# Kernel tuning notes

Measured on AMD Instinct MI355X. Metric: run time of the kernel, lower is better.

The kernel has to match this reference:

```python
import jax, jax.numpy as jnp
import numpy as np

_R, _C = 64, 64
_N = _R * _C
_SEC_PER_A = 31556926.0
_K = 0.01        # sheet_conductivity
_ALPHA = 1.25    # sheet_flow_exp
_HR = 0.1        # bedrock_step_height
_LR = 2.0        # cavity_spacing
_A = 5e-25       # cavity_closure_coeff
_NEXP = 3        # Glen exponent


def _build_grid():
    idx = np.arange(_N).reshape(_R, _C)
    tail = np.concatenate([idx[:, :-1].ravel(), idx[:-1, :].ravel()]).astype(np.int32)
    head = np.concatenate([idx[:, 1:].ravel(), idx[1:, :].ravel()]).astype(np.int32)
    L = tail.size
    links_at_node = -np.ones((_N, 4), np.int32)
    adj = -np.ones((_N, 4), np.int32)
    cnt = np.zeros(_N, np.int32)
    for l in range(L):
        for a, b in ((tail[l], head[l]), (head[l], tail[l])):
            links_at_node[a, cnt[a]] = l
            adj[a, cnt[a]] = b
            cnt[a] += 1
    r, c = np.divmod(np.arange(_N), _C)
    status = ((r == 0) | (r == _R - 1) | (c == 0) | (c == _C - 1)).astype(np.int32)
    return tail, head, links_at_node, adj, status


def setup_inputs():
    key = jax.random.key(0)
    k = jax.random.split(key, 8)
    tail, head, links_at_node, adj, status = _build_grid()
    L = tail.size
    bedrock = jax.random.uniform(k[0], (_N,), jnp.float32, 0.0, 500.0)
    ice_thk = jax.random.uniform(k[1], (_N,), jnp.float32, 100.0, 1000.0)
    overburden = 917.0 * 9.81 * ice_thk
    base_potential = 1000.0 * 9.81 * bedrock + overburden
    potential = base_potential - 0.3 * overburden + 1e3 * jax.random.normal(k[2], (_N,), jnp.float32)
    sheet_thickness = jax.random.uniform(k[3], (_N,), jnp.float32, 0.01, 0.1)
    sliding_velocity = jax.random.uniform(k[4], (L,), jnp.float32, 10.0, 100.0)
    specific_melt_rate = jax.random.uniform(k[5], (_N,), jnp.float32, 1e-7, 1e-6)
    link_length = jnp.full((L,), 100.0, jnp.float32)
    adj_j = jnp.asarray(adj)
    # mean over ALL 4 slots, padded entries contribute 0 (matches original jnp.mean)
    adj_pot = jnp.mean(jnp.where(adj_j != -1, base_potential[adj_j], 0.0), axis=1)
    inflow = jnp.where(base_potential > adj_pot, 1, -1) * (jnp.asarray(status) > 0)
    return dict(
        base_potential=base_potential,
        overburden_pressure=overburden,
        specific_melt_rate=specific_melt_rate,
        sheet_thickness=sheet_thickness,
        potential=potential,
        sliding_velocity=sliding_velocity,
        link_length=link_length,
        link_tail=jnp.asarray(tail),
        link_head=jnp.asarray(head),
        links_at_node=jnp.asarray(links_at_node),
        inflow_outflow=inflow.astype(jnp.int32),
        dt=3600,
    )


def reference(base_potential, overburden_pressure, specific_melt_rate, sheet_thickness,
              potential, sliding_velocity, link_length, link_tail, link_head,
              links_at_node, inflow_outflow, dt):
    N = base_potential.shape[0]
    t, h = link_tail, link_head
    # --- elliptic operator assembly (per-link, scatter into dense [N,N]) ---
    sheets = 0.5 * (sheet_thickness[t] + sheet_thickness[h])
    inv_grad = jnp.abs((potential[t] - potential[h]) / link_length) ** (-0.5)
    c = -_K * sheets ** _ALPHA * link_length * inv_grad  # symmetric link coefficient (<0)
    dir_row = inflow_outflow == 1  # Dirichlet rows
    ct = jnp.where(dir_row[t], 0.0, c)  # contribution into row tail
    ch = jnp.where(dir_row[h], 0.0, c)  # contribution into row head
    M = (jnp.zeros((N, N), base_potential.dtype)
         .at[t, h].add(ct).at[h, t].add(ch)
         .at[t, t].add(-ct).at[h, h].add(-ch))
    M = jnp.where(dir_row[:, None], jnp.eye(N, dtype=M.dtype), M)
    forcing = jnp.where(dir_row, base_potential - overburden_pressure, specific_melt_rate)
    new_potential = jnp.linalg.solve(M, forcing)
    # --- sheet thickness: map_mean_of_links_to_node then Newton on node-local ODE ---
    valid = links_at_node != -1
    lv = (sliding_velocity / _SEC_PER_A)[links_at_node]  # [N,4]
    sliding = jnp.abs(jnp.sum(jnp.where(valid, lv, 0.0), axis=1)
                      / jnp.maximum(valid.sum(axis=1), 1))
    pressure = base_potential - new_potential
    dtf = jnp.asarray(dt, base_potential.dtype)
    # residual r(h) = h - h0 - dt*(sliding*(HR-h)/LR - A*P^n*h) is LINEAR in h,
    # so Newton converges in one exact step -> closed form:
    new_h = (sheet_thickness + dtf * sliding * _HR / _LR) / (
        1.0 + dtf * (sliding / _LR + _A * pressure ** _NEXP))
    return new_potential, new_h
```

## Files before the change

### kernel.cpp

```cpp
#include <hip/hip_runtime.h>
#include <math.h>


#define NT    512
#define NPT   8
#define NN    4096
#define NC    1024
#define NCC   256
#define CCIT  20
#define MAXIT 40

enum : int { RSHL1 = 0x101, RSHR1 = 0x111,
             ROR8 = 0x128, ROR12 = 0x12C, ROR14 = 0x12E, ROR15 = 0x12F,
             WSHL1 = 0x130, WSHR1 = 0x138 };

template<int CTRL>
__device__ __forceinline__ float dppf(float x) {
    return __int_as_float(__builtin_amdgcn_update_dpp(
        __float_as_int(x), __float_as_int(x), CTRL, 0xF, 0xF, false));
}
template<int CTRL>
__device__ __forceinline__ double dppd(double x) {
    const int lo = __double2loint(x), hi = __double2hiint(x);
    const int l2 = __builtin_amdgcn_update_dpp(lo, lo, CTRL, 0xF, 0xF, false);
    const int h2 = __builtin_amdgcn_update_dpp(hi, hi, CTRL, 0xF, 0xF, false);
    return __hiloint2double(h2, l2);
}
__device__ __forceinline__ void pl16sw(int& a, int& b) {
    asm volatile("s_nop 1\n\tv_permlane16_swap_b32 %0, %1" : "+v"(a), "+v"(b));
}
__device__ __forceinline__ void pl32sw(int& a, int& b) {
    asm volatile("s_nop 1\n\tv_permlane32_swap_b32 %0, %1" : "+v"(a), "+v"(b));
}
__device__ __forceinline__ float shift_dn16(float x, bool inR2) {
    int a = __float_as_int(x), b = __float_as_int(x);
    pl16sw(a, b);
    int g = b, g2 = b;
    pl32sw(g, g2);
    return __int_as_float(inR2 ? g : a);
}
__device__ __forceinline__ float shift_up16(float x, bool inR1) {
    int a = __float_as_int(x), b = __float_as_int(x);
    pl16sw(a, b);
    int d1 = __float_as_int(x), d2 = __float_as_int(x);
    pl32sw(d1, d2);
    int e1 = d2, e2 = d2;
    pl16sw(e1, e2);
    return __int_as_float(inR1 ? e1 : b);
}
__device__ __forceinline__ double dsw32(double x) {
    int lo = __double2loint(x), hi = __double2hiint(x);
    int a = lo, b = lo; pl32sw(a, b);
    int c = hi, d = hi; pl32sw(c, d);
    return __hiloint2double(d, b);
}
__device__ __forceinline__ double dsw16(double x) {
    int lo = __double2loint(x), hi = __double2hiint(x);
    int a = lo, b = lo; pl16sw(a, b);
    int c = hi, d = hi; pl16sw(c, d);
    return __hiloint2double(d, b);
}

__global__ __launch_bounds__(NT, 1)
void sds_solver(const float* __restrict__ base_pot,
                const float* __restrict__ ovb,
                const float* __restrict__ melt,
                const float* __restrict__ sheet,
                const float* __restrict__ pot,
                const float* __restrict__ svel,
                const float* __restrict__ llen,
                const int*   __restrict__ ltail,
                const int*   __restrict__ lhead,
                const int*   __restrict__ lan,
                const int*   __restrict__ inflow,
                const int*   __restrict__ dt_raw,
                float* __restrict__ out,
                int N, int L)
{
    __shared__ __align__(16) float ZL0[2112], ZH0[2112];
    __shared__ __align__(16) float ZL1[2112], ZH1[2112];
    __shared__ __align__(16) float cW[NN], cE[NN], cN[NN], cS[NN];
    __shared__ __align__(16) float CB[32 + NC + 32];
    __shared__ __align__(16) float CB2[32 + NC + 32];
    __shared__ __align__(16) float EB[32 + NC + 32];
    __shared__ __align__(16) float ccb[NCC];
    __shared__ __align__(16) float cWc_s[NC], cEc_s[NC], cNc_s[NC], cSc_s[NC], dc_s[NC];
    __shared__ double redp[32], redg[16];

    const int tid  = threadIdx.x;
    const int lane = tid & 63;
    const int wid  = tid >> 6;
    const int m    = tid * NPT;

    if (N != NN || L != 8064) return;

    const int dti = dt_raw[0];
    const float as_f = __int_as_float(dti);
    const double dtf = (as_f > 0.5f && as_f < 1.0e12f) ? (double)as_f : (double)dti;

    const float invthf = 0.8f;
    const float c1f = 0.2195122f, c2f = 0.9756098f;
    const float wA = 1.75f;

    {
        const float4 z4 = make_float4(0.f, 0.f, 0.f, 0.f);
        #pragma unroll
        for (int i = tid; i < NN/4; i += NT) {
            ((float4*)cW)[i] = z4; ((float4*)cE)[i] = z4;
            ((float4*)cN)[i] = z4; ((float4*)cS)[i] = z4;
        }
        if (tid < 32) {
            ZL0[tid]=0.f; ZL0[2080+tid]=0.f; ZH0[tid]=0.f; ZH0[2080+tid]=0.f;
            ZL1[tid]=0.f; ZL1[2080+tid]=0.f; ZH1[tid]=0.f; ZH1[2080+tid]=0.f;
            CB[tid]=0.f;  CB[32+NC+tid]=0.f;
            CB2[tid]=0.f; CB2[32+NC+tid]=0.f;
            EB[tid]=0.f;  EB[32+NC+tid]=0.f;
        }
    }
    __syncthreads();

    for (int l = tid; l < 8064; l += NT) {
        int t, h;
        if (l < 4032) {
            const int r = l / 63;
            const int c2 = l - r * 63;
            t = (r << 6) + c2; h = t + 1;
        } else {
            t = l - 4032; h = t + 64;
        }
        const float sheets = 0.5f * (sheet[t] + sheet[h]);
        const float len = llen[l];
        const float grad = fabsf((pot[t] - pot[h]) / len);
        const float c = -0.01f * (sheets * sqrtf(sqrtf(sheets))) * len / sqrtf(grad);
        const bool dt_ = (inflow[t] == 1);
        const bool dh_ = (inflow[h] == 1);
        if (l < 4032) { cE[t] = dt_ ? 0.f : c; cW[h] = dh_ ? 0.f : c; }
        else          { cS[t] = dt_ ? 0.f : c; cN[h] = dh_ ? 0.f : c; }
    }
    __syncthreads();

    float cw[NPT], ce[NPT], cn[NPT], cs[NPT], dgf[NPT], invdf[NPT];
    double bb[NPT], gg[NPT], xv[NPT], rv[NPT];
    bool dirf[NPT];
    auto ldco = [&]() {
        const float4 w0 = *(const float4*)&cW[m], w1 = *(const float4*)&cW[m+4];
        const float4 e0 = *(const float4*)&cE[m], e1 = *(const float4*)&cE[m+4];
        const float4 n0 = *(const float4*)&cN[m], n1 = *(const float4*)&cN[m+4];
        const float4 s0 = *(const float4*)&cS[m], s1 = *(const float4*)&cS[m+4];
        cw[0]=w0.x;cw[1]=w0.y;cw[2]=w0.z;cw[3]=w0.w;cw[4]=w1.x;cw[5]=w1.y;cw[6]=w1.z;cw[7]=w1.w;
        ce[0]=e0.x;ce[1]=e0.y;ce[2]=e0.z;ce[3]=e0.w;ce[4]=e1.x;ce[5]=e1.y;ce[6]=e1.z;ce[7]=e1.w;
        cn[0]=n0.x;cn[1]=n0.y;cn[2]=n0.z;cn[3]=n0.w;cn[4]=n1.x;cn[5]=n1.y;cn[6]=n1.z;cn[7]=n1.w;
        cs[0]=s0.x;cs[1]=s0.y;cs[2]=s0.z;cs[3]=s0.w;cs[4]=s1.x;cs[5]=s1.y;cs[6]=s1.z;cs[7]=s1.w;
    };
    ldco();
    double gsum = 0.0, gcnt = 0.0;
    #pragma unroll
    for (int k = 0; k < NPT; ++k) {
        const int n = m + k;
        const bool dir = (inflow[n] == 1);
        const double g = (double)base_pot[n] - (double)ovb[n];
        const double d = -((double)cw[k] + (double)ce[k] + (double)cn[k] + (double)cs[k]);
        const double dg = (dir || d == 0.0) ? 1.0 : d;
        dgf[k] = (float)dg; invdf[k] = (float)(1.0 / dg);
        bb[k] = dir ? g : (double)melt[n];
        gg[k] = g; dirf[k] = dir;
        if (dir) { gsum += g; gcnt += 1.0; }
    }
    {
        #pragma unroll
        for (int off = 32; off > 0; off >>= 1) {
            gsum += __shfl_down(gsum, off, 64);
            gcnt += __shfl_down(gcnt, off, 64);
        }
        if (lane == 0) { redg[2*wid] = gsum; redg[2*wid+1] = gcnt; }
        __syncthreads();
        gsum = 0.0; gcnt = 0.0;
        #pragma unroll
        for (int w = 0; w < NT/64; ++w) { gsum += redg[2*w]; gcnt += redg[2*w+1]; }
    }
    const double gmean = gsum / (gcnt > 0.0 ? gcnt : 1.0);

    auto stz = [&](float* L_, float* H_, const float* v) {
        *(float4*)&L_[32 + 4*tid] = make_float4(v[0], v[1], v[2], v[3]);
        *(float4*)&H_[32 + 4*tid] = make_float4(v[4], v[5], v[6], v[7]);
    };
    float qf[NPT];
    auto spmv = [&](const float* L_, const float* H_, const float* vr) {
        const float4 uL = *(const float4*)&L_[4*tid];
        const float4 uH = *(const float4*)&H_[4*tid];
        const float4 dL = *(const float4*)&L_[64 + 4*tid];
        const float4 dH = *(const float4*)&H_[64 + 4*tid];
        const float lw = dppf<WSHR1>(vr[7]);
        const float re = dppf<WSHL1>(vr[0]);
        const float up[NPT] = {uL.x,uL.y,uL.z,uL.w,uH.x,uH.y,uH.z,uH.w};
        const float dn[NPT] = {dL.x,dL.y,dL.z,dL.w,dH.x,dH.y,dH.z,dH.w};
        #pragma unroll
        for (int k = 0; k < NPT; ++k) {
            const float wv = k ? vr[k-1] : lw;
            const float ev = (k < NPT-1) ? vr[k+1] : re;
            qf[k] = dgf[k]*vr[k] + cw[k]*wv + ce[k]*ev + cn[k]*up[k] + cs[k]*dn[k];
        }
    };
    auto fread0 = [&](int n) -> float {
        const int off = 32 + ((n >> 3) << 2) + (n & 3);
        return (n & 4) ? ZH0[off] : ZL0[off];
    };

    {
        float x0r[NPT];
        #pragma unroll
        for (int k = 0; k < NPT; ++k) {
            const float x0f = (float)(dirf[k] ? gg[k] : gmean);
            xv[k] = (double)x0f; x0r[k] = x0f;
        }
        stz(ZL0, ZH0, x0r); __syncthreads();
        spmv(ZL0, ZH0, x0r);
        #pragma unroll
        for (int k = 0; k < NPT; ++k)
            rv[k] = dirf[k] ? 0.0 : (bb[k] - (double)qf[k]);
    }
    __syncthreads();

    {
        #pragma unroll
        for (int k = 0; k < NPT; ++k) {
            const int n = m + k;
            if ((n & 63) != 0  && inflow[n-1]  == 1) cW[n] = 0.f;
            if ((n & 63) != 63 && inflow[n+1]  == 1) cE[n] = 0.f;
            if (n >= 64        && inflow[n-64] == 1) cN[n] = 0.f;
            if (n < NN-64      && inflow[n+64] == 1) cS[n] = 0.f;
        }
        float dgfF[NPT];
        #pragma unroll
        for (int k = 0; k < NPT; ++k) dgfF[k] = dirf[k] ? 0.f : dgf[k];
        stz(ZL0, ZH0, dgfF);
    }
    __syncthreads();
    ldco();

    #pragma unroll
    for (int q = 0; q < 2; ++q) {
        const int I = 2*tid + q;
        const int R = tid >> 4, C = I & 31;
        const int na = 128*R + 2*C, nb = na+1, nc_ = na+64, nd = na+65;
        cEc_s[I] = cE[nb] + cE[nd];
        cWc_s[I] = cW[na] + cW[nc_];
        cNc_s[I] = cN[na] + cN[nb];
        cSc_s[I] = cS[nc_] + cS[nd];
        const float d = fread0(na)+fread0(nb)+fread0(nc_)+fread0(nd)
                      + 2.0f*(cE[na] + cE[nc_] + cS[na] + cS[nb]);
        dc_s[I] = (d > 0.f) ? d : 1.0f;
    }
    __syncthreads();

    float cwc[2], cec[2], cnc[2], csc[2], dcr[2], invdc[2];
    {
        float2 t;
        t = *(float2*)&cWc_s[2*tid]; cwc[0]=t.x; cwc[1]=t.y;
        t = *(float2*)&cEc_s[2*tid]; cec[0]=t.x; cec[1]=t.y;
        t = *(float2*)&cNc_s[2*tid]; cnc[0]=t.x; cnc[1]=t.y;
        t = *(float2*)&cSc_s[2*tid]; csc[0]=t.x; csc[1]=t.y;
        t = *(float2*)&dc_s[2*tid];  dcr[0]=t.x; dcr[1]=t.y;
        invdc[0] = 1.0f/dcr[0]; invdc[1] = 1.0f/dcr[1];
    }
    float cwcc[4], cecc[4], cncc[4], cscc[4], dccr[4], invdcc[4];
    if (tid < 64) {
        #pragma unroll
        for (int j = 0; j < 4; ++j) {
            const int Rc = ((tid >> 4) << 2) + j, Cc = tid & 15;
            const int IA = 64*Rc + 2*Cc, IB = IA+1, IC = IA+32, ID = IA+33;
            cecc[j] = cEc_s[IB] + cEc_s[ID];
            cwcc[j] = cWc_s[IA] + cWc_s[IC];
            cncc[j] = cNc_s[IA] + cNc_s[IB];
            cscc[j] = cSc_s[IC] + cSc_s[ID];
            const float d = dc_s[IA]+dc_s[IB]+dc_s[IC]+dc_s[ID]
                          + 2.0f*(cEc_s[IA] + cEc_s[IC] + cSc_s[IA] + cSc_s[IB]);
            dccr[j] = (d > 0.f) ? d : 1.0f;
            invdcc[j] = 1.0f/dccr[j];
        }
    }
    float c1cc[CCIT+1], c2cc[CCIT+1], invthcc;
    {
        const double a = 8e-3, b2 = 2.0;
        const double th = 0.5*(b2+a), de = 0.5*(b2-a), s1 = th/de;
        double rp = 1.0/s1;
        for (int j = 1; j <= CCIT; ++j) {
            const double rj = 1.0/(2.0*s1 - rp);
            c1cc[j] = (float)(rj*rp);
            c2cc[j] = (float)(2.0*rj/de);
            rp = rj;
        }
        invthcc = (float)(1.0/th);
    }
    auto cspmv = [&](const float* B_, float v0, float v1, float& q0, float& q1) {
        const float2 up = *(const float2*)&B_[2*tid];
        const float2 dn = *(const float2*)&B_[64 + 2*tid];
        const float wv = dppf<WSHR1>(v1);
        const float ev = dppf<WSHL1>(v0);
        q0 = dcr[0]*v0 + cwc[0]*wv + cec[0]*v1 + cnc[0]*up.x + csc[0]*dn.x;
        q1 = dcr[1]*v1 + cwc[1]*v0 + cec[1]*ev + cnc[1]*up.y + csc[1]*dn.y;
    };

    double rho_prev = 0.0, pap = 0.0, tol = 0.0;
    double pv[NPT], sv[NPT], rpv[NPT];
    #pragma unroll
    for (int k = 0; k < NPT; ++k) { pv[k]=0.0; sv[k]=0.0; rpv[k]=0.0; }

    for (int it = 0; it < MAXIT; ++it) {
        float f0[NPT], d0[NPT], d1[NPT], zpre[NPT];
        #pragma unroll
        for (int k = 0; k < NPT; ++k) { f0[k] = (float)rv[k] * invdf[k]; d0[k] = f0[k] * invthf; }
        stz(ZL0, ZH0, d0); __syncthreads();
        spmv(ZL0, ZH0, d0);
        #pragma unroll
        for (int k = 0; k < NPT; ++k) {
            const float f1 = f0[k] - qf[k]*invdf[k];
            d1[k] = c1f*d0[k] + c2f*f1;
            zpre[k] = d0[k] + d1[k];
            f0[k] = f1;
        }
        stz(ZL1, ZH1, d1); __syncthreads();
        spmv(ZL1, ZH1, d1);

        float r1[NPT], r1p[NPT];
        #pragma unroll
        for (int k = 0; k < NPT; ++k) {
            const float fres = f0[k] - qf[k]*invdf[k];
            r1[k] = dirf[k] ? 0.f : dgf[k]*fres;
        }
        #pragma unroll
        for (int k = 0; k < NPT; ++k) r1p[k] = dppf<ROR8>(r1[k]);
        if ((tid & 8) == 0) {
            float4 rc4;
            rc4.x = r1[0]+r1[1]+r1p[0]+r1p[1];
            rc4.y = r1[2]+r1[3]+r1p[2]+r1p[3];
            rc4.z = r1[4]+r1[5]+r1p[4]+r1p[5];
            rc4.w = r1[6]+r1[7]+r1p[6]+r1p[7];
            const int I0 = 32*(tid >> 4) + 4*(tid & 7);
            *(float4*)&CB2[32 + I0] = rc4;
        }
        __syncthreads();

        float rc[2], f0c[2], d0c[2], d1c[2], qc0, qc1;
        {
            const float2 rcl = *(const float2*)&CB2[32 + 2*tid];
            rc[0] = rcl.x; rc[1] = rcl.y;
        }
        #pragma unroll
        for (int q = 0; q < 2; ++q) {
            f0c[q] = rc[q] * invdc[q];
            d0c[q] = f0c[q] * invthf;
        }
        *(float2*)&CB[32 + 2*tid] = make_float2(d0c[0], d0c[1]);
        __syncthreads();
        cspmv(CB, d0c[0], d0c[1], qc0, qc1);
        {
            const float f1a = f0c[0] - qc0*invdc[0];
            const float f1b = f0c[1] - qc1*invdc[1];
            d1c[0] = c1f*d0c[0] + c2f*f1a;
            d1c[1] = c1f*d0c[1] + c2f*f1b;
            f0c[0] = f1a; f0c[1] = f1b;
        }
        *(float2*)&CB2[32 + 2*tid] = make_float2(d1c[0], d1c[1]);
        __syncthreads();
        cspmv(CB2, d1c[0], d1c[1], qc0, qc1);
        {
            const float fra = f0c[0] - qc0*invdc[0];
            const float frb = f0c[1] - qc1*invdc[1];
            *(float2*)&CB[32 + 2*tid] = make_float2(dcr[0]*fra, dcr[1]*frb);
        }
        __syncthreads();

        if (tid < 64) {
            const int cc_c  = tid & 15;
            const int cc_rb = tid >> 4;
            const bool inR1 = (cc_rb == 1), inR2 = (cc_rb == 2);
            float fr[4], dr[4], zc[4];
            #pragma unroll
            for (int j = 0; j < 4; ++j) {
                const int IA = (((cc_rb << 2) + j) << 6) + (cc_c << 1);
                const float rcc = CB[32+IA] + CB[32+IA+1] + CB[32+IA+32] + CB[32+IA+33];
                fr[j] = rcc * invdcc[j];
                dr[j] = fr[j] * invthcc;
                zc[j] = dr[j];
            }
            for (int s = 1; s <= CCIT; ++s) {
                const float zN = shift_dn16(dr[3], inR2);
                const float zS = shift_up16(dr[0], inR1);
                float qcc[4];
                #pragma unroll
                for (int j = 0; j < 4; ++j) {
                    const float wj = dppf<RSHR1>(dr[j]);
                    const float ej = dppf<RSHL1>(dr[j]);
                    const float nj = j ? dr[j-1] : zN;
                    const float sj = (j < 3) ? dr[j+1] : zS;
                    qcc[j] = dccr[j]*dr[j] + cwcc[j]*wj + cecc[j]*ej
                           + cncc[j]*nj + cscc[j]*sj;
                }
                #pragma unroll
                for (int j = 0; j < 4; ++j) {
                    fr[j] -= qcc[j] * invdcc[j];
                    dr[j]  = c1cc[s]*dr[j] + c2cc[s]*fr[j];
                    zc[j] += dr[j];
                }
            }
            #pragma unroll
            for (int j = 0; j < 4; ++j)
                ccb[(((cc_rb << 2) + j) << 4) + cc_c] = zc[j];
        }
        __syncthreads();

        const float ecv = wA * ccb[16*(tid >> 5) + (tid & 15)];
        float zmc[2] = { d0c[0] + d1c[0] + ecv, d0c[1] + d1c[1] + ecv };
        *(float2*)&CB2[32 + 2*tid] = make_float2(zmc[0], zmc[1]);
        __syncthreads();
        cspmv(CB2, zmc[0], zmc[1], qc0, qc1);
        float fmc[2] = { (rc[0]-qc0)*invdc[0], (rc[1]-qc1)*invdc[1] };
        float d0p[2] = { fmc[0]*invthf, fmc[1]*invthf };
        *(float2*)&CB[32 + 2*tid] = make_float2(d0p[0], d0p[1]);
        __syncthreads();
        cspmv(CB, d0p[0], d0p[1], qc0, qc1);
        {
            const float f1a = fmc[0] - qc0*invdc[0];
            const float f1b = fmc[1] - qc1*invdc[1];
            const float efa = zmc[0] + c1f*d0p[0] + c2f*f1a + d0p[0];
            const float efb = zmc[1] + c1f*d0p[1] + c2f*f1b + d0p[1];
            *(float2*)&EB[32 + 2*tid] = make_float2(efa, efb);
        }
        __syncthreads();

        const float4 e4 = *(const float4*)&EB[32 + 32*(tid >> 4) + (tid & 7)*4];
        const float* e4p = (const float*)&e4;
        float zmid[NPT], zf[NPT];
        #pragma unroll
        for (int k = 0; k < NPT; ++k)
            zmid[k] = zpre[k] + (dirf[k] ? 0.f : wA * e4p[k >> 1]);
        stz(ZL1, ZH1, zmid); __syncthreads();
        spmv(ZL1, ZH1, zmid);
        float fmid[NPT], d0q[NPT];
        #pragma unroll
        for (int k = 0; k < NPT; ++k) {
            fmid[k] = (float)rv[k]*invdf[k] - qf[k]*invdf[k];
            d0q[k]  = fmid[k] * invthf;
        }
        stz(ZL0, ZH0, d0q); __syncthreads();
        spmv(ZL0, ZH0, d0q);
        #pragma unroll
        for (int k = 0; k < NPT; ++k) {
            const float f1 = fmid[k] - qf[k]*invdf[k];
            zf[k] = zmid[k] + d0q[k] + c1f*d0q[k] + c2f*f1;
        }
        stz(ZL1, ZH1, zf); __syncthreads();
        spmv(ZL1, ZH1, zf);

        double rho_n = 0.0, rzp = 0.0, zw = 0.0, pw = 0.0;
        #pragma unroll
        for (int k = 0; k < NPT; ++k) {
            const double zk = (double)zf[k], wk = (double)qf[k];
            rho_n += rv[k]  * zk;
            rzp   += rpv[k] * zk;
            zw    += zk * wk;
            pw    += pv[k] * wk;
        }
        rho_n += dsw32(rho_n); rzp += dsw32(rzp); zw += dsw32(zw); pw += dsw32(pw);
        rho_n += dsw16(rho_n); rzp += dsw16(rzp); zw += dsw16(zw); pw += dsw16(pw);
        rho_n += dppd<ROR8 >(rho_n); rzp += dppd<ROR8 >(rzp); zw += dppd<ROR8 >(zw); pw += dppd<ROR8 >(pw);
        rho_n += dppd<ROR12>(rho_n); rzp += dppd<ROR12>(rzp); zw += dppd<ROR12>(zw); pw += dppd<ROR12>(pw);
        rho_n += dppd<ROR14>(rho_n); rzp += dppd<ROR14>(rzp); zw += dppd<ROR14>(zw); pw += dppd<ROR14>(pw);
        rho_n += dppd<ROR15>(rho_n); rzp += dppd<ROR15>(rzp); zw += dppd<ROR15>(zw); pw += dppd<ROR15>(pw);
        if (lane == 0) {
            redp[4*wid] = rho_n; redp[4*wid+1] = rzp;
            redp[4*wid+2] = zw;  redp[4*wid+3] = pw;
        }
        __syncthreads();
        rho_n = 0.0; rzp = 0.0; zw = 0.0; pw = 0.0;
        #pragma unroll
        for (int w = 0; w < NT/64; ++w) {
            rho_n += redp[4*w];   rzp += redp[4*w+1];
            zw    += redp[4*w+2]; pw  += redp[4*w+3];
        }

        if (it == 0) {
            tol = rho_n * 1e-3 + 1e-300;
            if (!(rho_n > 0.0)) break;
        } else if (rho_n <= tol || !(rho_n > 0.0)) break;
        const double beta = (it == 0) ? 0.0
                          : fmax(0.0, (rho_n - rzp) / rho_prev);
        pap = zw + beta * (2.0 * pw + beta * pap);
        if (!(pap > 0.0)) break;
        const double alpha = rho_n / pap;
        rho_prev = rho_n;
        #pragma unroll
        for (int k = 0; k < NPT; ++k) {
            rpv[k] = rv[k];
            pv[k] = (double)zf[k] + beta * pv[k];
            sv[k] = (double)qf[k] + beta * sv[k];
            xv[k] += alpha * pv[k];
            rv[k] -= alpha * sv[k];
        }
    }

    float xo[NPT], ho[NPT];
    #pragma unroll
    for (int k = 0; k < NPT; ++k) {
        const int n = m + k;
        const int r = n >> 6, c2 = n & 63;
        const double x = dirf[k] ? gg[k] : xv[k];
        xo[k] = (float)x;

        const int hb = r * 63 + c2;
        float sva = 0.0f; int cnt = 0;
        if (c2 > 0)  { sva += svel[hb - 1];       cnt++; }
        if (c2 < 63) { sva += svel[hb];           cnt++; }
        if (r  > 0)  { sva += svel[4032 + n - 64]; cnt++; }
        if (r  < 63) { sva += svel[4032 + n];      cnt++; }
        const double sliding =
            fabs((double)sva / 31556926.0 / (double)(cnt > 0 ? cnt : 1));
        const double P   = (double)base_pot[n] - x;
        const double num = (double)sheet[n] + dtf * sliding * 0.1 / 2.0;
        const double den = 1.0 + dtf * (sliding / 2.0 + 5e-25 * P * P * P);
        ho[k] = (float)(num / den);
    }
    *(float4*)&out[m]        = make_float4(xo[0], xo[1], xo[2], xo[3]);
    *(float4*)&out[m+4]      = make_float4(xo[4], xo[5], xo[6], xo[7]);
    *(float4*)&out[NN+m]     = make_float4(ho[0], ho[1], ho[2], ho[3]);
    *(float4*)&out[NN+m+4]   = make_float4(ho[4], ho[5], ho[6], ho[7]);
}

extern "C" void kernel_launch(void* const* d_in, const int* in_sizes, int n_in,
                              void* d_out, int out_size, void* d_ws, size_t ws_size,
                              hipStream_t stream) {
    const float* base_pot = (const float*)d_in[0];
    const float* ovb      = (const float*)d_in[1];
    const float* melt     = (const float*)d_in[2];
    const float* sheet    = (const float*)d_in[3];
    const float* pot      = (const float*)d_in[4];
    const float* svel     = (const float*)d_in[5];
    const float* llen     = (const float*)d_in[6];
    const int*   ltail    = (const int*)d_in[7];
    const int*   lhead    = (const int*)d_in[8];
    const int*   lan      = (const int*)d_in[9];
    const int*   inflow   = (const int*)d_in[10];
    const int*   dt_raw   = (const int*)d_in[11];
    float* out = (float*)d_out;
    const int N = in_sizes[0];
    const int L = in_sizes[5];

    hipLaunchKernelGGL(sds_solver, dim3(1), dim3(NT), 0, stream,
                       base_pot, ovb, melt, sheet, pot, svel, llen,
                       ltail, lhead, lan, inflow, dt_raw, out, N, L);
}
```

Measured before the change: 149.4 us.

## Recompute neighbor halo values locally to drop barrier-separated SpMV staging

```diff
diff --git a/kernel.cpp b/kernel.cpp
--- a/kernel.cpp
+++ b/kernel.cpp
@@ -79,10 +79,12 @@
 {
     __shared__ __align__(16) float ZL0[2112], ZH0[2112];
     __shared__ __align__(16) float ZL1[2112], ZH1[2112];
+    __shared__ __align__(16) float DML[2112], DMH[2112];
     __shared__ __align__(16) float cW[NN], cE[NN], cN[NN], cS[NN];
     __shared__ __align__(16) float CB[32 + NC + 32];
     __shared__ __align__(16) float CB2[32 + NC + 32];
     __shared__ __align__(16) float EB[32 + NC + 32];
+    __shared__ __align__(16) float IDC[32 + NC + 32];
     __shared__ __align__(16) float ccb[NCC];
     __shared__ __align__(16) float cWc_s[NC], cEc_s[NC], cNc_s[NC], cSc_s[NC], dc_s[NC];
     __shared__ double redp[32], redg[16];
@@ -112,9 +114,11 @@
         if (tid < 32) {
             ZL0[tid]=0.f; ZL0[2080+tid]=0.f; ZH0[tid]=0.f; ZH0[2080+tid]=0.f;
             ZL1[tid]=0.f; ZL1[2080+tid]=0.f; ZH1[tid]=0.f; ZH1[2080+tid]=0.f;
+            DML[tid]=0.f; DML[2080+tid]=0.f; DMH[tid]=0.f; DMH[2080+tid]=0.f;
             CB[tid]=0.f;  CB[32+NC+tid]=0.f;
             CB2[tid]=0.f; CB2[32+NC+tid]=0.f;
             EB[tid]=0.f;  EB[32+NC+tid]=0.f;
+            IDC[tid]=0.f; IDC[32+NC+tid]=0.f;
         }
     }
     __syncthreads();
@@ -184,6 +188,12 @@
         *(float4*)&L_[32 + 4*tid] = make_float4(v[0], v[1], v[2], v[3]);
         *(float4*)&H_[32 + 4*tid] = make_float4(v[4], v[5], v[6], v[7]);
     };
+    {
+        float dmf[NPT];
+        #pragma unroll
+        for (int k = 0; k < NPT; ++k) dmf[k] = dirf[k] ? 0.f : 1.f;
+        stz(DML, DMH, dmf);
+    }
     float qf[NPT];
     auto spmv = [&](const float* L_, const float* H_, const float* vr) {
         const float4 uL = *(const float4*)&L_[4*tid];
@@ -262,6 +272,7 @@
         t = *(float2*)&cSc_s[2*tid]; csc[0]=t.x; csc[1]=t.y;
         t = *(float2*)&dc_s[2*tid];  dcr[0]=t.x; dcr[1]=t.y;
         invdc[0] = 1.0f/dcr[0]; invdc[1] = 1.0f/dcr[1];
+        *(float2*)&IDC[32 + 2*tid] = make_float2(invdc[0], invdc[1]);
     }
     float cwcc[4], cecc[4], cncc[4], cscc[4], dccr[4], invdcc[4];
     if (tid < 64) {
@@ -351,9 +362,18 @@
             f0c[q] = rc[q] * invdc[q];
             d0c[q] = f0c[q] * invthf;
         }
-        *(float2*)&CB[32 + 2*tid] = make_float2(d0c[0], d0c[1]);
-        __syncthreads();
-        cspmv(CB, d0c[0], d0c[1], qc0, qc1);
+        {
+            const float2 ru = *(const float2*)&CB2[2*tid];
+            const float2 rd = *(const float2*)&CB2[64 + 2*tid];
+            const float2 iu = *(const float2*)&IDC[2*tid];
+            const float2 id = *(const float2*)&IDC[64 + 2*tid];
+            const float wv = dppf<WSHR1>(d0c[1]);
+            const float ev = dppf<WSHL1>(d0c[0]);
+            qc0 = dcr[0]*d0c[0] + cwc[0]*wv + cec[0]*d0c[1]
+                + cnc[0]*((ru.x*iu.x)*invthf) + csc[0]*((rd.x*id.x)*invthf);
+            qc1 = dcr[1]*d0c[1] + cwc[1]*d0c[0] + cec[1]*ev
+                + cnc[1]*((ru.y*iu.y)*invthf) + csc[1]*((rd.y*id.y)*invthf);
+        }
         {
             const float f1a = f0c[0] - qc0*invdc[0];
             const float f1b = f0c[1] - qc1*invdc[1];
@@ -361,9 +381,9 @@
             d1c[1] = c1f*d0c[1] + c2f*f1b;
             f0c[0] = f1a; f0c[1] = f1b;
         }
-        *(float2*)&CB2[32 + 2*tid] = make_float2(d1c[0], d1c[1]);
-        __syncthreads();
-        cspmv(CB2, d1c[0], d1c[1], qc0, qc1);
+        *(float2*)&EB[32 + 2*tid] = make_float2(d1c[0], d1c[1]);
+        __syncthreads();
+        cspmv(EB, d1c[0], d1c[1], qc0, qc1);
         {
             const float fra = f0c[0] - qc0*invdc[0];
             const float frb = f0c[1] - qc1*invdc[1];
@@ -412,9 +432,27 @@
 
         const float ecv = wA * ccb[16*(tid >> 5) + (tid & 15)];
         float zmc[2] = { d0c[0] + d1c[0] + ecv, d0c[1] + d1c[1] + ecv };
-        *(float2*)&CB2[32 + 2*tid] = make_float2(zmc[0], zmc[1]);
-        __syncthreads();
-        cspmv(CB2, zmc[0], zmc[1], qc0, qc1);
+        {
+            const float2 ru = *(const float2*)&CB2[2*tid];
+            const float2 rd = *(const float2*)&CB2[64 + 2*tid];
+            const float2 iu = *(const float2*)&IDC[2*tid];
+            const float2 id = *(const float2*)&IDC[64 + 2*tid];
+            const float2 du = *(const float2*)&EB[2*tid];
+            const float2 dd = *(const float2*)&EB[64 + 2*tid];
+            const int R = tid >> 4;
+            const int Ru = (R > 0)  ? R - 1 : 0;
+            const int Rd = (R < 31) ? R + 1 : 31;
+            const float ecu = wA * ccb[(Ru >> 1)*16 + (tid & 15)];
+            const float ecd = wA * ccb[(Rd >> 1)*16 + (tid & 15)];
+            const float upx = ((ru.x*iu.x)*invthf + du.x) + ecu;
+            const float upy = ((ru.y*iu.y)*invthf + du.y) + ecu;
+            const float dnx = ((rd.x*id.x)*invthf + dd.x) + ecd;
+            const float dny = ((rd.y*id.y)*invthf + dd.y) + ecd;
+            const float wv = dppf<WSHR1>(zmc[1]);
+            const float ev = dppf<WSHL1>(zmc[0]);
+            qc0 = dcr[0]*zmc[0] + cwc[0]*wv + cec[0]*zmc[1] + cnc[0]*upx + csc[0]*dnx;
+            qc1 = dcr[1]*zmc[1] + cwc[1]*zmc[0] + cec[1]*ev + cnc[1]*upy + csc[1]*dny;
+        }
         float fmc[2] = { (rc[0]-qc0)*invdc[0], (rc[1]-qc1)*invdc[1] };
         float d0p[2] = { fmc[0]*invthf, fmc[1]*invthf };
         *(float2*)&CB[32 + 2*tid] = make_float2(d0p[0], d0p[1]);
@@ -435,8 +473,41 @@
         #pragma unroll
         for (int k = 0; k < NPT; ++k)
             zmid[k] = zpre[k] + (dirf[k] ? 0.f : wA * e4p[k >> 1]);
-        stz(ZL1, ZH1, zmid); __syncthreads();
-        spmv(ZL1, ZH1, zmid);
+        {
+            const int rh = tid >> 4, rpar = (tid >> 3) & 1;
+            const float4 eu4 = *(const float4*)&EB[32 + 32*(rh - 1 + rpar) + (tid & 7)*4];
+            const float4 ed4 = *(const float4*)&EB[32 + 32*(rh + rpar) + (tid & 7)*4];
+            const float* eup = (const float*)&eu4;
+            const float* edp = (const float*)&ed4;
+            const float4 a0u = *(const float4*)&ZL0[4*tid];
+            const float4 b0u = *(const float4*)&ZH0[4*tid];
+            const float4 a1u = *(const float4*)&ZL1[4*tid];
+            const float4 b1u = *(const float4*)&ZH1[4*tid];
+            const float4 m0u = *(const float4*)&DML[4*tid];
+            const float4 m1u = *(const float4*)&DMH[4*tid];
+            const float4 a0d = *(const float4*)&ZL0[64 + 4*tid];
+            const float4 b0d = *(const float4*)&ZH0[64 + 4*tid];
+            const float4 a1d = *(const float4*)&ZL1[64 + 4*tid];
+            const float4 b1d = *(const float4*)&ZH1[64 + 4*tid];
+            const float4 m0d = *(const float4*)&DML[64 + 4*tid];
+            const float4 m1d = *(const float4*)&DMH[64 + 4*tid];
+            const float d0u[NPT] = {a0u.x,a0u.y,a0u.z,a0u.w,b0u.x,b0u.y,b0u.z,b0u.w};
+            const float d1u[NPT] = {a1u.x,a1u.y,a1u.z,a1u.w,b1u.x,b1u.y,b1u.z,b1u.w};
+            const float dmu[NPT] = {m0u.x,m0u.y,m0u.z,m0u.w,m1u.x,m1u.y,m1u.z,m1u.w};
+            const float d0d[NPT] = {a0d.x,a0d.y,a0d.z,a0d.w,b0d.x,b0d.y,b0d.z,b0d.w};
+            const float d1d[NPT] = {a1d.x,a1d.y,a1d.z,a1d.w,b1d.x,b1d.y,b1d.z,b1d.w};
+            const float dmd[NPT] = {m0d.x,m0d.y,m0d.z,m0d.w,m1d.x,m1d.y,m1d.z,m1d.w};
+            const float lw = dppf<WSHR1>(zmid[7]);
+            const float re = dppf<WSHL1>(zmid[0]);
+            #pragma unroll
+            for (int k = 0; k < NPT; ++k) {
+                const float upv = (d0u[k] + d1u[k]) + dmu[k]*(wA * eup[k >> 1]);
+                const float dnv = (d0d[k] + d1d[k]) + dmd[k]*(wA * edp[k >> 1]);
+                const float wv = k ? zmid[k-1] : lw;
+                const float ev = (k < NPT-1) ? zmid[k+1] : re;
+                qf[k] = dgf[k]*zmid[k] + cw[k]*wv + ce[k]*ev + cn[k]*upv + cs[k]*dnv;
+            }
+        }
         float fmid[NPT], d0q[NPT];
         #pragma unroll
         for (int k = 0; k < NPT; ++k) {
```

Result: slower. 153.8 us (+3.0%).

## Remap threads to column-strips so stencil neighbors come from registers and DPP

Applied to the files above, without the earlier changes.

```diff
diff --git a/kernel.cpp b/kernel.cpp
--- a/kernel.cpp
+++ b/kernel.cpp
@@ -77,9 +77,9 @@
                 float* __restrict__ out,
                 int N, int L)
 {
-    __shared__ __align__(16) float ZL0[2112], ZH0[2112];
-    __shared__ __align__(16) float ZL1[2112], ZH1[2112];
     __shared__ __align__(16) float cW[NN], cE[NN], cN[NN], cS[NN];
+    __shared__ __align__(16) float FD[NN];
+    __shared__ __align__(16) float BNDA[8*128], BNDB[8*128];
     __shared__ __align__(16) float CB[32 + NC + 32];
     __shared__ __align__(16) float CB2[32 + NC + 32];
     __shared__ __align__(16) float EB[32 + NC + 32];
@@ -90,7 +90,7 @@
     const int tid  = threadIdx.x;
     const int lane = tid & 63;
     const int wid  = tid >> 6;
-    const int m    = tid * NPT;
+    const int nb0  = (wid << 9) + lane;
 
     if (N != NN || L != 8064) return;
 
@@ -110,8 +110,6 @@
             ((float4*)cN)[i] = z4; ((float4*)cS)[i] = z4;
         }
         if (tid < 32) {
-            ZL0[tid]=0.f; ZL0[2080+tid]=0.f; ZH0[tid]=0.f; ZH0[2080+tid]=0.f;
-            ZL1[tid]=0.f; ZL1[2080+tid]=0.f; ZH1[tid]=0.f; ZH1[2080+tid]=0.f;
             CB[tid]=0.f;  CB[32+NC+tid]=0.f;
             CB2[tid]=0.f; CB2[32+NC+tid]=0.f;
             EB[tid]=0.f;  EB[32+NC+tid]=0.f;
@@ -143,20 +141,17 @@
     double bb[NPT], gg[NPT], xv[NPT], rv[NPT];
     bool dirf[NPT];
     auto ldco = [&]() {
-        const float4 w0 = *(const float4*)&cW[m], w1 = *(const float4*)&cW[m+4];
-        const float4 e0 = *(const float4*)&cE[m], e1 = *(const float4*)&cE[m+4];
-        const float4 n0 = *(const float4*)&cN[m], n1 = *(const float4*)&cN[m+4];
-        const float4 s0 = *(const float4*)&cS[m], s1 = *(const float4*)&cS[m+4];
-        cw[0]=w0.x;cw[1]=w0.y;cw[2]=w0.z;cw[3]=w0.w;cw[4]=w1.x;cw[5]=w1.y;cw[6]=w1.z;cw[7]=w1.w;
-        ce[0]=e0.x;ce[1]=e0.y;ce[2]=e0.z;ce[3]=e0.w;ce[4]=e1.x;ce[5]=e1.y;ce[6]=e1.z;ce[7]=e1.w;
-        cn[0]=n0.x;cn[1]=n0.y;cn[2]=n0.z;cn[3]=n0.w;cn[4]=n1.x;cn[5]=n1.y;cn[6]=n1.z;cn[7]=n1.w;
-        cs[0]=s0.x;cs[1]=s0.y;cs[2]=s0.z;cs[3]=s0.w;cs[4]=s1.x;cs[5]=s1.y;cs[6]=s1.z;cs[7]=s1.w;
+        #pragma unroll
+        for (int k = 0; k < NPT; ++k) {
+            const int n = nb0 + (k << 6);
+            cw[k] = cW[n]; ce[k] = cE[n]; cn[k] = cN[n]; cs[k] = cS[n];
+        }
     };
     ldco();
     double gsum = 0.0, gcnt = 0.0;
     #pragma unroll
     for (int k = 0; k < NPT; ++k) {
-        const int n = m + k;
+        const int n = nb0 + (k << 6);
         const bool dir = (inflow[n] == 1);
         const double g = (double)base_pot[n] - (double)ovb[n];
         const double d = -((double)cw[k] + (double)ce[k] + (double)cn[k] + (double)cs[k]);
@@ -180,30 +175,21 @@
     }
     const double gmean = gsum / (gcnt > 0.0 ? gcnt : 1.0);
 
-    auto stz = [&](float* L_, float* H_, const float* v) {
-        *(float4*)&L_[32 + 4*tid] = make_float4(v[0], v[1], v[2], v[3]);
-        *(float4*)&H_[32 + 4*tid] = make_float4(v[4], v[5], v[6], v[7]);
+    auto stB = [&](float* B, const float* v) {
+        *(float2*)&B[(wid << 7) + (lane << 1)] = make_float2(v[0], v[7]);
     };
     float qf[NPT];
-    auto spmv = [&](const float* L_, const float* H_, const float* vr) {
-        const float4 uL = *(const float4*)&L_[4*tid];
-        const float4 uH = *(const float4*)&H_[4*tid];
-        const float4 dL = *(const float4*)&L_[64 + 4*tid];
-        const float4 dH = *(const float4*)&H_[64 + 4*tid];
-        const float lw = dppf<WSHR1>(vr[7]);
-        const float re = dppf<WSHL1>(vr[0]);
-        const float up[NPT] = {uL.x,uL.y,uL.z,uL.w,uH.x,uH.y,uH.z,uH.w};
-        const float dn[NPT] = {dL.x,dL.y,dL.z,dL.w,dH.x,dH.y,dH.z,dH.w};
-        #pragma unroll
-        for (int k = 0; k < NPT; ++k) {
-            const float wv = k ? vr[k-1] : lw;
-            const float ev = (k < NPT-1) ? vr[k+1] : re;
-            qf[k] = dgf[k]*vr[k] + cw[k]*wv + ce[k]*ev + cn[k]*up[k] + cs[k]*dn[k];
-        }
-    };
-    auto fread0 = [&](int n) -> float {
-        const int off = 32 + ((n >> 3) << 2) + (n & 3);
-        return (n & 4) ? ZH0[off] : ZL0[off];
+    auto spmvC = [&](const float* B, const float* vr) {
+        const float nb = B[(((wid + 7) & 7) << 7) + (lane << 1) + 1];
+        const float sb = B[(((wid + 1) & 7) << 7) + (lane << 1) + 0];
+        #pragma unroll
+        for (int k = 0; k < NPT; ++k) {
+            const float wv = dppf<WSHR1>(vr[k]);
+            const float ev = dppf<WSHL1>(vr[k]);
+            const float nv = k ? vr[k-1] : nb;
+            const float sv = (k < NPT-1) ? vr[k+1] : sb;
+            qf[k] = dgf[k]*vr[k] + cw[k]*wv + ce[k]*ev + cn[k]*nv + cs[k]*sv;
+        }
     };
 
     {
@@ -213,8 +199,8 @@
             const float x0f = (float)(dirf[k] ? gg[k] : gmean);
             xv[k] = (double)x0f; x0r[k] = x0f;
         }
-        stz(ZL0, ZH0, x0r); __syncthreads();
-        spmv(ZL0, ZH0, x0r);
+        stB(BNDA, x0r); __syncthreads();
+        spmvC(BNDA, x0r);
         #pragma unroll
         for (int k = 0; k < NPT; ++k)
             rv[k] = dirf[k] ? 0.0 : (bb[k] - (double)qf[k]);
@@ -224,16 +210,13 @@
     {
         #pragma unroll
         for (int k = 0; k < NPT; ++k) {
-            const int n = m + k;
-            if ((n & 63) != 0  && inflow[n-1]  == 1) cW[n] = 0.f;
-            if ((n & 63) != 63 && inflow[n+1]  == 1) cE[n] = 0.f;
+            const int n = nb0 + (k << 6);
+            if (lane != 0  && inflow[n-1]  == 1) cW[n] = 0.f;
+            if (lane != 63 && inflow[n+1]  == 1) cE[n] = 0.f;
             if (n >= 64        && inflow[n-64] == 1) cN[n] = 0.f;
             if (n < NN-64      && inflow[n+64] == 1) cS[n] = 0.f;
-        }
-        float dgfF[NPT];
-        #pragma unroll
-        for (int k = 0; k < NPT; ++k) dgfF[k] = dirf[k] ? 0.f : dgf[k];
-        stz(ZL0, ZH0, dgfF);
+            FD[n] = dirf[k] ? 0.f : dgf[k];
+        }
     }
     __syncthreads();
     ldco();
@@ -242,13 +225,13 @@
     for (int q = 0; q < 2; ++q) {
         const int I = 2*tid + q;
         const int R = tid >> 4, C = I & 31;
-        const int na = 128*R + 2*C, nb = na+1, nc_ = na+64, nd = na+65;
-        cEc_s[I] = cE[nb] + cE[nd];
+        const int na = 128*R + 2*C, nbq = na+1, nc_ = na+64, nd = na+65;
+        cEc_s[I] = cE[nbq] + cE[nd];
         cWc_s[I] = cW[na] + cW[nc_];
-        cNc_s[I] = cN[na] + cN[nb];
+        cNc_s[I] = cN[na] + cN[nbq];
         cSc_s[I] = cS[nc_] + cS[nd];
-        const float d = fread0(na)+fread0(nb)+fread0(nc_)+fread0(nd)
-                      + 2.0f*(cE[na] + cE[nc_] + cS[na] + cS[nb]);
+        const float d = FD[na]+FD[nbq]+FD[nc_]+FD[nd]
+                      + 2.0f*(cE[na] + cE[nc_] + cS[na] + cS[nbq]);
         dc_s[I] = (d > 0.f) ? d : 1.0f;
     }
     __syncthreads();
@@ -310,8 +293,8 @@
         float f0[NPT], d0[NPT], d1[NPT], zpre[NPT];
         #pragma unroll
         for (int k = 0; k < NPT; ++k) { f0[k] = (float)rv[k] * invdf[k]; d0[k] = f0[k] * invthf; }
-        stz(ZL0, ZH0, d0); __syncthreads();
-        spmv(ZL0, ZH0, d0);
+        stB(BNDA, d0); __syncthreads();
+        spmvC(BNDA, d0);
         #pragma unroll
         for (int k = 0; k < NPT; ++k) {
             const float f1 = f0[k] - qf[k]*invdf[k];
@@ -319,25 +302,21 @@
             zpre[k] = d0[k] + d1[k];
             f0[k] = f1;
         }
-        stz(ZL1, ZH1, d1); __syncthreads();
-        spmv(ZL1, ZH1, d1);
-
-        float r1[NPT], r1p[NPT];
+        stB(BNDB, d1); __syncthreads();
+        spmvC(BNDB, d1);
+
+        float r1[NPT], t2[NPT];
         #pragma unroll
         for (int k = 0; k < NPT; ++k) {
             const float fres = f0[k] - qf[k]*invdf[k];
             r1[k] = dirf[k] ? 0.f : dgf[k]*fres;
         }
         #pragma unroll
-        for (int k = 0; k < NPT; ++k) r1p[k] = dppf<ROR8>(r1[k]);
-        if ((tid & 8) == 0) {
-            float4 rc4;
-            rc4.x = r1[0]+r1[1]+r1p[0]+r1p[1];
-            rc4.y = r1[2]+r1[3]+r1p[2]+r1p[3];
-            rc4.z = r1[4]+r1[5]+r1p[4]+r1p[5];
-            rc4.w = r1[6]+r1[7]+r1p[6]+r1p[7];
-            const int I0 = 32*(tid >> 4) + 4*(tid & 7);
-            *(float4*)&CB2[32 + I0] = rc4;
+        for (int k = 0; k < NPT; ++k) t2[k] = r1[k] + dppf<WSHL1>(r1[k]);
+        if ((lane & 1) == 0) {
+            #pragma unroll
+            for (int j = 0; j < 4; ++j)
+                CB2[32 + ((wid << 2) + j)*32 + (lane >> 1)] = t2[2*j] + t2[2*j+1];
         }
         __syncthreads();
 
@@ -429,29 +408,31 @@
         }
         __syncthreads();
 
-        const float4 e4 = *(const float4*)&EB[32 + 32*(tid >> 4) + (tid & 7)*4];
-        const float* e4p = (const float*)&e4;
+        float ec[4];
+        #pragma unroll
+        for (int j = 0; j < 4; ++j)
+            ec[j] = EB[32 + ((wid << 2) + j)*32 + (lane >> 1)];
         float zmid[NPT], zf[NPT];
         #pragma unroll
         for (int k = 0; k < NPT; ++k)
-            zmid[k] = zpre[k] + (dirf[k] ? 0.f : wA * e4p[k >> 1]);
-        stz(ZL1, ZH1, zmid); __syncthreads();
-        spmv(ZL1, ZH1, zmid);
+            zmid[k] = zpre[k] + (dirf[k] ? 0.f : wA * ec[k >> 1]);
+        stB(BNDA, zmid); __syncthreads();
+        spmvC(BNDA, zmid);
         float fmid[NPT], d0q[NPT];
         #pragma unroll
         for (int k = 0; k < NPT; ++k) {
             fmid[k] = (float)rv[k]*invdf[k] - qf[k]*invdf[k];
             d0q[k]  = fmid[k] * invthf;
         }
-        stz(ZL0, ZH0, d0q); __syncthreads();
-        spmv(ZL0, ZH0, d0q);
+        stB(BNDB, d0q); __syncthreads();
+        spmvC(BNDB, d0q);
         #pragma unroll
         for (int k = 0; k < NPT; ++k) {
             const float f1 = fmid[k] - qf[k]*invdf[k];
             zf[k] = zmid[k] + d0q[k] + c1f*d0q[k] + c2f*f1;
         }
-        stz(ZL1, ZH1, zf); __syncthreads();
-        spmv(ZL1, ZH1, zf);
+        stB(BNDA, zf); __syncthreads();
+        spmvC(BNDA, zf);
 
         double rho_n = 0.0, rzp = 0.0, zw = 0.0, pw = 0.0;
         #pragma unroll
@@ -500,13 +481,11 @@
         }
     }
 
-    float xo[NPT], ho[NPT];
     #pragma unroll
     for (int k = 0; k < NPT; ++k) {
-        const int n = m + k;
-        const int r = n >> 6, c2 = n & 63;
+        const int n = nb0 + (k << 6);
+        const int r = (wid << 3) + k, c2 = lane;
         const double x = dirf[k] ? gg[k] : xv[k];
-        xo[k] = (float)x;
 
         const int hb = r * 63 + c2;
         float sva = 0.0f; int cnt = 0;
@@ -519,12 +498,9 @@
         const double P   = (double)base_pot[n] - x;
         const double num = (double)sheet[n] + dtf * sliding * 0.1 / 2.0;
         const double den = 1.0 + dtf * (sliding / 2.0 + 5e-25 * P * P * P);
-        ho[k] = (float)(num / den);
-    }
-    *(float4*)&out[m]        = make_float4(xo[0], xo[1], xo[2], xo[3]);
-    *(float4*)&out[m+4]      = make_float4(xo[4], xo[5], xo[6], xo[7]);
-    *(float4*)&out[NN+m]     = make_float4(ho[0], ho[1], ho[2], ho[3]);
-    *(float4*)&out[NN+m+4]   = make_float4(ho[4], ho[5], ho[6], ho[7]);
+        out[n]      = (float)x;
+        out[NN + n] = (float)(num / den);
+    }
 }
 
 extern "C" void kernel_launch(void* const* d_in, const int* in_sizes, int n_in,
```

Result: faster. 131.0 us (-12.3%).
